# Performance work log

Hardware: AMD Instinct MI355X
Metric: run time of the kernel (lower is better)

Reference implementation:

```python
import jax, jax.numpy as jnp
import numpy as np

N_EMBED = 1024
EMBED_DIM = 64
BETA = 0.25


def setup_inputs() -> dict:
    key = jax.random.key(0)
    k1, k2 = jax.random.split(key)
    x = jax.random.normal(k1, (32, EMBED_DIM, 64, 64), dtype=jnp.float32)  # NCHW, C == embed_dim
    embed = jax.random.uniform(
        k2, (N_EMBED, EMBED_DIM), dtype=jnp.float32,
        minval=-1.0 / N_EMBED, maxval=1.0 / N_EMBED,
    )
    return {"x": x, "embed": embed}


def reference(x, embed):
    # NCHW -> NHWC, flatten spatial+batch to rows of embed_dim
    z = jnp.transpose(x, (0, 2, 3, 1))                      # [B,H,W,D]
    zf = z.reshape(-1, EMBED_DIM)                           # [N,D]
    # squared L2 distance to every codeword: ||z||^2 + ||e||^2 - 2 z.e
    dist = (
        jnp.sum(zf * zf, axis=1, keepdims=True)
        + jnp.sum(embed * embed, axis=1)
        - 2.0 * zf @ embed.T
    )                                                       # [N, n_embed]
    idx = jnp.argmin(dist, axis=1)                          # [N]
    # one-hot @ embed == direct gather (same math, no scatter/matmul)
    z_q = embed[idx].reshape(z.shape)                       # [B,H,W,D]
    sg = jax.lax.stop_gradient
    loss = jnp.mean((sg(z_q) - z) ** 2) + BETA * jnp.mean((z_q - sg(z)) ** 2)
    # straight-through estimator
    z_q = z + sg(z_q - z)
    z_q = jnp.transpose(z_q, (0, 3, 1, 2))                  # back to NCHW
    return (z_q, loss)
```

## Files before the change

### kernel.cpp

```cpp
#include <hip/hip_runtime.h>


#define TOTAL_ELEMS 8388608
#define LOSS_SCALE (1.25f / 8388608.f)

typedef float  f32x4  __attribute__((ext_vector_type(4)));
typedef unsigned int u32x4 __attribute__((ext_vector_type(4)));
typedef long   longx2 __attribute__((ext_vector_type(2)));

static __device__ __forceinline__ void gload_lds16(const void* g, void* l) {
    __builtin_amdgcn_global_load_lds(
        (const __attribute__((address_space(1))) void*)g,
        (__attribute__((address_space(3))) void*)l,
        16, 0, 0);
}

static __device__ __forceinline__ unsigned int umax(unsigned int a, unsigned int b) {
    return a > b ? a : b;
}

__global__ void vq_prep(const float* __restrict__ embed,
                        unsigned char* __restrict__ eb,
                        float* __restrict__ c0,
                        float* __restrict__ loss_slot) {
    int t   = blockIdx.x * 256 + threadIdx.x;
    int row = t >> 2, qd = t & 3;
    const float* s0 = embed + row * 64 + qd * 8;
    const float* s1 = embed + row * 64 + 32 + qd * 8;
    f32x4 v0 = *(const f32x4*)s0, v1 = *(const f32x4*)(s0 + 4);
    f32x4 w0 = *(const f32x4*)s1, w1 = *(const f32x4*)(s1 + 4);
    float s = v0[0]*v0[0] + v0[1]*v0[1] + v0[2]*v0[2] + v0[3]*v0[3]
            + v1[0]*v1[0] + v1[1]*v1[1] + v1[2]*v1[2] + v1[3]*v1[3]
            + w0[0]*w0[0] + w0[1]*w0[1] + w0[2]*w0[2] + w0[3]*w0[3]
            + w1[0]*w1[0] + w1[1]*w1[1] + w1[2]*w1[2] + w1[3]*w1[3];
    unsigned int d0 = 0, d1 = 0, d2 = 0, d3 = 0;
    d0 = __builtin_amdgcn_cvt_pk_fp8_f32(v0[0]*1024.f, v0[1]*1024.f, d0, false);
    d0 = __builtin_amdgcn_cvt_pk_fp8_f32(v0[2]*1024.f, v0[3]*1024.f, d0, true);
    d1 = __builtin_amdgcn_cvt_pk_fp8_f32(v1[0]*1024.f, v1[1]*1024.f, d1, false);
    d1 = __builtin_amdgcn_cvt_pk_fp8_f32(v1[2]*1024.f, v1[3]*1024.f, d1, true);
    d2 = __builtin_amdgcn_cvt_pk_fp8_f32(w0[0]*1024.f, w0[1]*1024.f, d2, false);
    d2 = __builtin_amdgcn_cvt_pk_fp8_f32(w0[2]*1024.f, w0[3]*1024.f, d2, true);
    d3 = __builtin_amdgcn_cvt_pk_fp8_f32(w1[0]*1024.f, w1[1]*1024.f, d3, false);
    d3 = __builtin_amdgcn_cvt_pk_fp8_f32(w1[2]*1024.f, w1[3]*1024.f, d3, true);
    u32x4 o = {d0, d1, d2, d3};
    *(u32x4*)((char*)eb + row * 64 + qd * 16) = o;
    s += __shfl_xor(s, 1);
    s += __shfl_xor(s, 2);
    if (qd == 0) c0[row] = 64.f - 512.f * s;
    if (t == 0) *loss_slot = 0.f;
}

__global__ __launch_bounds__(256, 2) void vq_main(
    const float* __restrict__ x,
    const float* __restrict__ embed,
    const unsigned char* __restrict__ eb,
    const float* __restrict__ c0,
    float* __restrict__ out,
    float* __restrict__ loss) {

    __shared__ __align__(16) unsigned char cb[65536];
    __shared__ __align__(16) float c0l[1024];
    __shared__ float lpart[4];

    const int t    = threadIdx.x;
    const int wv   = t >> 6, lane = t & 63;
    const int l15  = lane & 15, lq = lane >> 4;

    const int blk = blockIdx.x;
    const int b   = blk >> 4;
    const int h0  = (blk & 15) * 4;
    const size_t xbase = (size_t)b * 262144 + (size_t)h0 * 64;

    const char* ebp = (const char*)eb;

#pragma unroll
    for (int s = 0; s < 16; s++)
        gload_lds16(ebp + s * 4096 + t * 16, &cb[s * 4096 + t * 16]);

    *(f32x4*)(c0l + t * 4) = *(const f32x4*)(c0 + t * 4);

    float part = 0.f;
    long bfr[4][2];
#pragma unroll
    for (int nt = 0; nt < 4; nt++) {
#pragma unroll
        for (int kh = 0; kh < 2; kh++) {
            unsigned int dw[2];
#pragma unroll
            for (int p = 0; p < 2; p++) {
                float f[4];
#pragma unroll
                for (int j = 0; j < 4; j++) {
                    f[j] = x[xbase + (size_t)(kh * 32 + lq * 8 + p * 4 + j) * 4096
                             + (size_t)wv * 64 + nt * 16 + l15];
                    part += f[j] * f[j];
                }
                unsigned int r = 0;
                r = __builtin_amdgcn_cvt_pk_fp8_f32(f[0], f[1], r, false);
                r = __builtin_amdgcn_cvt_pk_fp8_f32(f[2], f[3], r, true);
                dw[p] = r;
            }
            bfr[nt][kh] = (long)(((unsigned long long)dw[1] << 32) | dw[0]);
        }
    }
    __syncthreads();

    unsigned int key[4] = {0u, 0u, 0u, 0u};
    const unsigned char* abase = &cb[l15 * 64 + lq * 16];
    const float* cbase = c0l + lq * 4;
#pragma unroll 8
    for (int mt = 0; mt < 64; mt++) {
        longx2 av = *(const longx2*)(abase + mt * 1024);
        f32x4 c0v = *(const f32x4*)(cbase + mt * 16);
        const int invm = 1023 - mt * 16 - lq * 4;
#pragma unroll
        for (int nt = 0; nt < 4; nt++) {
            f32x4 acc = __builtin_amdgcn_mfma_f32_16x16x32_fp8_fp8(
                av[0], bfr[nt][0], c0v, 0, 0, 0);
            acc = __builtin_amdgcn_mfma_f32_16x16x32_fp8_fp8(
                av[1], bfr[nt][1], acc, 0, 0, 0);
            unsigned int k0 = (__float_as_uint(acc[0]) & 0xFFFFFC00u) | (unsigned int)(invm);
            unsigned int k1 = (__float_as_uint(acc[1]) & 0xFFFFFC00u) | (unsigned int)(invm - 1);
            unsigned int k2 = (__float_as_uint(acc[2]) & 0xFFFFFC00u) | (unsigned int)(invm - 2);
            unsigned int k3 = (__float_as_uint(acc[3]) & 0xFFFFFC00u) | (unsigned int)(invm - 3);
            key[nt] = umax(key[nt], umax(umax(k0, k1), umax(k2, k3)));
        }
    }

#pragma unroll
    for (int nt = 0; nt < 4; nt++) {
        unsigned int k = key[nt];
        unsigned int o = (unsigned int)__shfl_xor((int)k, 16); k = umax(k, o);
        o = (unsigned int)__shfl_xor((int)k, 32);              k = umax(k, o);
        key[nt] = k;
        part -= (1.f / 2048.f) * __uint_as_float(k & 0xFFFFFC00u);
    }

    unsigned int klo = (lane & 16) ? key[1] : key[0];
    unsigned int khi = (lane & 16) ? key[3] : key[2];
    unsigned int ks  = (lane & 32) ? khi : klo;
    const int idx = 1023 - (int)(ks & 1023u);

#pragma unroll
    for (int off = 1; off < 64; off <<= 1) part += __shfl_xor(part, off);
    if (lane == 0) lpart[wv] = part;

    const float* erow = embed + idx * 64;
    float* orow = out + xbase + (size_t)wv * 64 + lane;
#pragma unroll
    for (int c4 = 0; c4 < 16; c4++) {
        f32x4 ev = *(const f32x4*)(erow + c4 * 4);
#pragma unroll
        for (int j = 0; j < 4; j++)
            orow[(size_t)(c4 * 4 + j) * 4096] = ev[j];
    }

    __syncthreads();
    if (t == 0) {
        atomicAdd(loss, (lpart[0] + lpart[1] + lpart[2] + lpart[3] + 32.0f) * LOSS_SCALE);
    }
}

extern "C" void kernel_launch(void* const* d_in, const int* in_sizes, int n_in,
                              void* d_out, int out_size, void* d_ws, size_t ws_size,
                              hipStream_t stream) {
    const float* x     = (const float*)d_in[0];
    const float* embed = (const float*)d_in[1];
    unsigned char* eb  = (unsigned char*)d_ws;
    float* c0          = (float*)((char*)d_ws + 65536);
    float* out  = (float*)d_out;
    float* loss = out + TOTAL_ELEMS;

    vq_prep<<<16, 256, 0, stream>>>(embed, eb, c0, loss);
    vq_main<<<512, 256, 0, stream>>>(x, embed, eb, c0, out, loss);
}
```

Before: 37.06 us.

## Use 512-thread blocks and swap MFMA operands so codewords map to columns

Doubles the threads per block to 512, so each wave handles 32 positions instead of 64 while the block still shares one 64KB LDS codebook. The MFMA operand order is swapped so positions become rows and codewords become columns. The argmin then reduces across the 16 lanes with xor shuffles instead of across rows and quads. Indices go through shared memory, and the gather/write is split so each half-wave writes 32 channels. This adds an extra block barrier and more shuffle work, and relies on launch bounds of 4 blocks per CU to hold occupancy.

```diff
diff --git a/kernel.cpp b/kernel.cpp
--- a/kernel.cpp
+++ b/kernel.cpp
@@ -50,7 +50,7 @@
     if (t == 0) *loss_slot = 0.f;
 }
 
-__global__ __launch_bounds__(256, 2) void vq_main(
+__global__ __launch_bounds__(512, 4) void vq_main(
     const float* __restrict__ x,
     const float* __restrict__ embed,
     const unsigned char* __restrict__ eb,
@@ -60,7 +60,8 @@
 
     __shared__ __align__(16) unsigned char cb[65536];
     __shared__ __align__(16) float c0l[1024];
-    __shared__ float lpart[4];
+    __shared__ int   idxf[256];
+    __shared__ float lpart[8];
 
     const int t    = threadIdx.x;
     const int wv   = t >> 6, lane = t & 63;
@@ -70,19 +71,20 @@
     const int b   = blk >> 4;
     const int h0  = (blk & 15) * 4;
     const size_t xbase = (size_t)b * 262144 + (size_t)h0 * 64;
+    const int rowoff = (wv >> 1) * 64 + (wv & 1) * 32;
 
     const char* ebp = (const char*)eb;
 
 #pragma unroll
-    for (int s = 0; s < 16; s++)
-        gload_lds16(ebp + s * 4096 + t * 16, &cb[s * 4096 + t * 16]);
+    for (int s = 0; s < 8; s++)
+        gload_lds16(ebp + s * 8192 + t * 16, &cb[s * 8192 + t * 16]);
 
-    *(f32x4*)(c0l + t * 4) = *(const f32x4*)(c0 + t * 4);
+    if (t < 256) *(f32x4*)(c0l + t * 4) = *(const f32x4*)(c0 + t * 4);
 
     float part = 0.f;
-    long bfr[4][2];
+    long bfr[2][2];
 #pragma unroll
-    for (int nt = 0; nt < 4; nt++) {
+    for (int nt = 0; nt < 2; nt++) {
 #pragma unroll
         for (int kh = 0; kh < 2; kh++) {
             unsigned int dw[2];
@@ -92,7 +94,7 @@
 #pragma unroll
                 for (int j = 0; j < 4; j++) {
                     f[j] = x[xbase + (size_t)(kh * 32 + lq * 8 + p * 4 + j) * 4096
-                             + (size_t)wv * 64 + nt * 16 + l15];
+                             + (size_t)rowoff + nt * 16 + l15];
                     part += f[j] * f[j];
                 }
                 unsigned int r = 0;
@@ -105,59 +107,75 @@
     }
     __syncthreads();
 
-    unsigned int key[4] = {0u, 0u, 0u, 0u};
-    const unsigned char* abase = &cb[l15 * 64 + lq * 16];
-    const float* cbase = c0l + lq * 4;
+    unsigned int key[8];
+#pragma unroll
+    for (int s = 0; s < 8; s++) key[s] = 0u;
+    const unsigned char* bbase = &cb[l15 * 64 + lq * 16];
+    const float* cbase = c0l + l15;
+    const unsigned int invb = (unsigned int)(1023 - l15);
 #pragma unroll 8
     for (int mt = 0; mt < 64; mt++) {
-        longx2 av = *(const longx2*)(abase + mt * 1024);
-        f32x4 c0v = *(const f32x4*)(cbase + mt * 16);
-        const int invm = 1023 - mt * 16 - lq * 4;
+        longx2 bv = *(const longx2*)(bbase + mt * 1024);
+        float c0s = cbase[mt * 16];
+        f32x4 c0v = {c0s, c0s, c0s, c0s};
+        const unsigned int inv = invb - mt * 16;
 #pragma unroll
-        for (int nt = 0; nt < 4; nt++) {
+        for (int nt = 0; nt < 2; nt++) {
             f32x4 acc = __builtin_amdgcn_mfma_f32_16x16x32_fp8_fp8(
-                av[0], bfr[nt][0], c0v, 0, 0, 0);
+                bfr[nt][0], bv[0], c0v, 0, 0, 0);
             acc = __builtin_amdgcn_mfma_f32_16x16x32_fp8_fp8(
-                av[1], bfr[nt][1], acc, 0, 0, 0);
-            unsigned int k0 = (__float_as_uint(acc[0]) & 0xFFFFFC00u) | (unsigned int)(invm);
-            unsigned int k1 = (__float_as_uint(acc[1]) & 0xFFFFFC00u) | (unsigned int)(invm - 1);
-            unsigned int k2 = (__float_as_uint(acc[2]) & 0xFFFFFC00u) | (unsigned int)(invm - 2);
-            unsigned int k3 = (__float_as_uint(acc[3]) & 0xFFFFFC00u) | (unsigned int)(invm - 3);
-            key[nt] = umax(key[nt], umax(umax(k0, k1), umax(k2, k3)));
+                bfr[nt][1], bv[1], acc, 0, 0, 0);
+#pragma unroll
+            for (int r = 0; r < 4; r++) {
+                unsigned int k2 = (__float_as_uint(acc[r]) & 0xFFFFFC00u) | inv;
+                key[nt * 4 + r] = umax(key[nt * 4 + r], k2);
+            }
         }
     }
 
 #pragma unroll
-    for (int nt = 0; nt < 4; nt++) {
-        unsigned int k = key[nt];
-        unsigned int o = (unsigned int)__shfl_xor((int)k, 16); k = umax(k, o);
-        o = (unsigned int)__shfl_xor((int)k, 32);              k = umax(k, o);
-        key[nt] = k;
-        part -= (1.f / 2048.f) * __uint_as_float(k & 0xFFFFFC00u);
+    for (int s = 0; s < 8; s++) {
+        unsigned int k = key[s];
+        k = umax(k, (unsigned int)__shfl_xor((int)k, 1));
+        k = umax(k, (unsigned int)__shfl_xor((int)k, 2));
+        k = umax(k, (unsigned int)__shfl_xor((int)k, 4));
+        k = umax(k, (unsigned int)__shfl_xor((int)k, 8));
+        key[s] = k;
     }
-
-    unsigned int klo = (lane & 16) ? key[1] : key[0];
-    unsigned int khi = (lane & 16) ? key[3] : key[2];
-    unsigned int ks  = (lane & 32) ? khi : klo;
-    const int idx = 1023 - (int)(ks & 1023u);
+    if (l15 == 0) {
+#pragma unroll
+        for (int nt = 0; nt < 2; nt++) {
+#pragma unroll
+            for (int r = 0; r < 4; r++) {
+                unsigned int k = key[nt * 4 + r];
+                idxf[rowoff + nt * 16 + lq * 4 + r] = 1023 - (int)(k & 1023u);
+                part -= (1.f / 512.f) * __uint_as_float(k & 0xFFFFFC00u);
+            }
+        }
+    }
 
 #pragma unroll
     for (int off = 1; off < 64; off <<= 1) part += __shfl_xor(part, off);
     if (lane == 0) lpart[wv] = part;
+    __syncthreads();
 
-    const float* erow = embed + idx * 64;
-    float* orow = out + xbase + (size_t)wv * 64 + lane;
+    const int ch0 = (lane >> 5) * 32;
+    const int pos = lane & 31;
+    const int idx = idxf[rowoff + pos];
+    const float* erow = embed + idx * 64 + ch0;
+    float* orow = out + xbase + (size_t)rowoff + pos + (size_t)ch0 * 4096;
 #pragma unroll
-    for (int c4 = 0; c4 < 16; c4++) {
+    for (int c4 = 0; c4 < 8; c4++) {
         f32x4 ev = *(const f32x4*)(erow + c4 * 4);
 #pragma unroll
         for (int j = 0; j < 4; j++)
             orow[(size_t)(c4 * 4 + j) * 4096] = ev[j];
     }
 
-    __syncthreads();
     if (t == 0) {
-        atomicAdd(loss, (lpart[0] + lpart[1] + lpart[2] + lpart[3] + 32.0f) * LOSS_SCALE);
+        float s = lpart[0] + lpart[1] + lpart[2] + lpart[3]
+                + lpart[4] + lpart[5] + lpart[6] + lpart[7];
+        atomicAdd(loss, (s + 32.0f) * LOSS_SCALE);
     }
 }
 
@@ -172,5 +190,5 @@
     float* loss = out + TOTAL_ELEMS;
 
     vq_prep<<<16, 256, 0, stream>>>(embed, eb, c0, loss);
-    vq_main<<<512, 256, 0, stream>>>(x, embed, eb, c0, out, loss);
+    vq_main<<<512, 512, 0, stream>>>(x, embed, eb, c0, out, loss);
 }
```

Result: no change. 37.53 us (+1.3%).

## Split codebook across waves per block, read fragments from global instead of LDS

Applied to the files above, without the earlier changes.

Each block now handles one 64-pixel row instead of four. The four waves split the 1024 codewords four ways and combine their argmin keys through shared memory, in place of each wave scanning the full codebook held in LDS. The prep kernel writes the fp8 codebook directly in MFMA fragment order, so the main kernel loads A operands straight from global/L2 without the 64KB LDS staging. The grid grows to 2048 blocks and launch bounds are removed. This drops LDS occupancy limits and per-block codebook staging, but every wave redundantly loads the same x tile and adds two block barriers plus a cross-wave reduction.

```diff
diff --git a/kernel.cpp b/kernel.cpp
--- a/kernel.cpp
+++ b/kernel.cpp
@@ -4,16 +4,7 @@
 #define TOTAL_ELEMS 8388608
 #define LOSS_SCALE (1.25f / 8388608.f)
 
-typedef float  f32x4  __attribute__((ext_vector_type(4)));
-typedef unsigned int u32x4 __attribute__((ext_vector_type(4)));
-typedef long   longx2 __attribute__((ext_vector_type(2)));
-
-static __device__ __forceinline__ void gload_lds16(const void* g, void* l) {
-    __builtin_amdgcn_global_load_lds(
-        (const __attribute__((address_space(1))) void*)g,
-        (__attribute__((address_space(3))) void*)l,
-        16, 0, 0);
-}
+typedef float f32x4 __attribute__((ext_vector_type(4)));
 
 static __device__ __forceinline__ unsigned int umax(unsigned int a, unsigned int b) {
     return a > b ? a : b;
@@ -25,6 +16,7 @@
                         float* __restrict__ loss_slot) {
     int t   = blockIdx.x * 256 + threadIdx.x;
     int row = t >> 2, qd = t & 3;
+    int mt  = row >> 4, rl = row & 15;
     const float* s0 = embed + row * 64 + qd * 8;
     const float* s1 = embed + row * 64 + 32 + qd * 8;
     f32x4 v0 = *(const f32x4*)s0, v1 = *(const f32x4*)(s0 + 4);
@@ -42,15 +34,18 @@
     d2 = __builtin_amdgcn_cvt_pk_fp8_f32(w0[2]*1024.f, w0[3]*1024.f, d2, true);
     d3 = __builtin_amdgcn_cvt_pk_fp8_f32(w1[0]*1024.f, w1[1]*1024.f, d3, false);
     d3 = __builtin_amdgcn_cvt_pk_fp8_f32(w1[2]*1024.f, w1[3]*1024.f, d3, true);
-    u32x4 o = {d0, d1, d2, d3};
-    *(u32x4*)((char*)eb + row * 64 + qd * 16) = o;
+    unsigned long long g0 = (unsigned long long)d0 | ((unsigned long long)d1 << 32);
+    unsigned long long g1 = (unsigned long long)d2 | ((unsigned long long)d3 << 32);
+    char* tb = (char*)eb + mt * 1024 + (qd * 16 + rl) * 8;
+    *(unsigned long long*)(tb)       = g0;
+    *(unsigned long long*)(tb + 512) = g1;
     s += __shfl_xor(s, 1);
     s += __shfl_xor(s, 2);
     if (qd == 0) c0[row] = 64.f - 512.f * s;
     if (t == 0) *loss_slot = 0.f;
 }
 
-__global__ __launch_bounds__(256, 2) void vq_main(
+__global__ void vq_main(
     const float* __restrict__ x,
     const float* __restrict__ embed,
     const unsigned char* __restrict__ eb,
@@ -58,26 +53,16 @@
     float* __restrict__ out,
     float* __restrict__ loss) {
 
-    __shared__ __align__(16) unsigned char cb[65536];
-    __shared__ __align__(16) float c0l[1024];
-    __shared__ float lpart[4];
+    __shared__ unsigned int wkey[4][64];
+    __shared__ int idxf[64];
 
     const int t    = threadIdx.x;
     const int wv   = t >> 6, lane = t & 63;
     const int l15  = lane & 15, lq = lane >> 4;
 
     const int blk = blockIdx.x;
-    const int b   = blk >> 4;
-    const int h0  = (blk & 15) * 4;
-    const size_t xbase = (size_t)b * 262144 + (size_t)h0 * 64;
-
-    const char* ebp = (const char*)eb;
-
-#pragma unroll
-    for (int s = 0; s < 16; s++)
-        gload_lds16(ebp + s * 4096 + t * 16, &cb[s * 4096 + t * 16]);
-
-    *(f32x4*)(c0l + t * 4) = *(const f32x4*)(c0 + t * 4);
+    const int b   = blk >> 6, h = blk & 63;
+    const size_t xbase = (size_t)b * 262144 + (size_t)h * 64;
 
     float part = 0.f;
     long bfr[4][2];
@@ -92,7 +77,7 @@
 #pragma unroll
                 for (int j = 0; j < 4; j++) {
                     f[j] = x[xbase + (size_t)(kh * 32 + lq * 8 + p * 4 + j) * 4096
-                             + (size_t)wv * 64 + nt * 16 + l15];
+                             + nt * 16 + l15];
                     part += f[j] * f[j];
                 }
                 unsigned int r = 0;
@@ -103,22 +88,29 @@
             bfr[nt][kh] = (long)(((unsigned long long)dw[1] << 32) | dw[0]);
         }
     }
-    __syncthreads();
+    float zsq = 0.f;
+    if (wv == 0) {
+#pragma unroll
+        for (int off = 1; off < 64; off <<= 1) part += __shfl_xor(part, off);
+        zsq = part;
+    }
 
     unsigned int key[4] = {0u, 0u, 0u, 0u};
-    const unsigned char* abase = &cb[l15 * 64 + lq * 16];
-    const float* cbase = c0l + lq * 4;
-#pragma unroll 8
-    for (int mt = 0; mt < 64; mt++) {
-        longx2 av = *(const longx2*)(abase + mt * 1024);
-        f32x4 c0v = *(const f32x4*)(cbase + mt * 16);
-        const int invm = 1023 - mt * 16 - lq * 4;
+    const char* ebq = (const char*)eb + wv * 16384 + lane * 8;
+    const float* c0q = c0 + wv * 256 + lq * 4;
+    const int invq = 1023 - wv * 256 - lq * 4;
+#pragma unroll 4
+    for (int m = 0; m < 16; m++) {
+        long a0 = *(const long*)(ebq + m * 1024);
+        long a1 = *(const long*)(ebq + m * 1024 + 512);
+        f32x4 c0v = *(const f32x4*)(c0q + m * 16);
+        const int invm = invq - m * 16;
 #pragma unroll
         for (int nt = 0; nt < 4; nt++) {
             f32x4 acc = __builtin_amdgcn_mfma_f32_16x16x32_fp8_fp8(
-                av[0], bfr[nt][0], c0v, 0, 0, 0);
+                a0, bfr[nt][0], c0v, 0, 0, 0);
             acc = __builtin_amdgcn_mfma_f32_16x16x32_fp8_fp8(
-                av[1], bfr[nt][1], acc, 0, 0, 0);
+                a1, bfr[nt][1], acc, 0, 0, 0);
             unsigned int k0 = (__float_as_uint(acc[0]) & 0xFFFFFC00u) | (unsigned int)(invm);
             unsigned int k1 = (__float_as_uint(acc[1]) & 0xFFFFFC00u) | (unsigned int)(invm - 1);
             unsigned int k2 = (__float_as_uint(acc[2]) & 0xFFFFFC00u) | (unsigned int)(invm - 2);
@@ -130,35 +122,36 @@
 #pragma unroll
     for (int nt = 0; nt < 4; nt++) {
         unsigned int k = key[nt];
-        unsigned int o = (unsigned int)__shfl_xor((int)k, 16); k = umax(k, o);
-        o = (unsigned int)__shfl_xor((int)k, 32);              k = umax(k, o);
-        key[nt] = k;
-        part -= (1.f / 2048.f) * __uint_as_float(k & 0xFFFFFC00u);
+        k = umax(k, (unsigned int)__shfl_xor((int)k, 16));
+        k = umax(k, (unsigned int)__shfl_xor((int)k, 32));
+        if (lane < 16) wkey[wv][nt * 16 + lane] = k;
     }
+    __syncthreads();
 
-    unsigned int klo = (lane & 16) ? key[1] : key[0];
-    unsigned int khi = (lane & 16) ? key[3] : key[2];
-    unsigned int ks  = (lane & 32) ? khi : klo;
-    const int idx = 1023 - (int)(ks & 1023u);
+    float la = 0.f;
+    if (t < 64) {
+        unsigned int k = umax(umax(wkey[0][t], wkey[1][t]),
+                              umax(wkey[2][t], wkey[3][t]));
+        idxf[t] = 1023 - (int)(k & 1023u);
+        la = -(1.f / 512.f) * __uint_as_float(k & 0xFFFFFC00u);
+#pragma unroll
+        for (int off = 1; off < 64; off <<= 1) la += __shfl_xor(la, off);
+    }
+    __syncthreads();
 
+    const int idx = idxf[lane];
+    const float* erow = embed + idx * 64 + wv * 16;
+    float* obase = out + xbase + (size_t)(wv * 16) * 4096 + lane;
 #pragma unroll
-    for (int off = 1; off < 64; off <<= 1) part += __shfl_xor(part, off);
-    if (lane == 0) lpart[wv] = part;
-
-    const float* erow = embed + idx * 64;
-    float* orow = out + xbase + (size_t)wv * 64 + lane;
-#pragma unroll
-    for (int c4 = 0; c4 < 16; c4++) {
+    for (int c4 = 0; c4 < 4; c4++) {
         f32x4 ev = *(const f32x4*)(erow + c4 * 4);
 #pragma unroll
         for (int j = 0; j < 4; j++)
-            orow[(size_t)(c4 * 4 + j) * 4096] = ev[j];
+            obase[(size_t)(c4 * 4 + j) * 4096] = ev[j];
     }
 
-    __syncthreads();
-    if (t == 0) {
-        atomicAdd(loss, (lpart[0] + lpart[1] + lpart[2] + lpart[3] + 32.0f) * LOSS_SCALE);
-    }
+    if (t == 0)
+        atomicAdd(loss, (zsq + la + 8.0f) * LOSS_SCALE);
 }
 
 extern "C" void kernel_launch(void* const* d_in, const int* in_sizes, int n_in,
@@ -172,5 +165,5 @@
     float* loss = out + TOTAL_ELEMS;
 
     vq_prep<<<16, 256, 0, stream>>>(embed, eb, c0, loss);
-    vq_main<<<512, 256, 0, stream>>>(x, embed, eb, c0, out, loss);
+    vq_main<<<2048, 256, 0, stream>>>(x, embed, eb, c0, out, loss);
 }
```

Result: slower. 45.95 us (+24.0%).

## Fuse codebook prep into main kernel with padded LDS rows and 512-thread blocks

Applied to the files above, without the earlier changes.

Removes the separate prep kernel: each block now reads the fp32 codebook, computes the norms and fp8-quantizes it straight into LDS, using 72-byte padded rows to avoid bank conflicts. Blocks grow to 512 threads (8 waves), each wave handling 32 positions instead of 64, which halves the per-wave MFMA work and the register footprint. The loss slot is zeroed with a memset instead. In exchange, all 512 blocks redo the codebook conversion, which adds redundant global reads and ALU work per block.

```diff
diff --git a/kernel.cpp b/kernel.cpp
--- a/kernel.cpp
+++ b/kernel.cpp
@@ -3,64 +3,27 @@
 
 #define TOTAL_ELEMS 8388608
 #define LOSS_SCALE (1.25f / 8388608.f)
+#define ROWB 72
 
-typedef float  f32x4  __attribute__((ext_vector_type(4)));
+typedef float  f32x4 __attribute__((ext_vector_type(4)));
 typedef unsigned int u32x4 __attribute__((ext_vector_type(4)));
-typedef long   longx2 __attribute__((ext_vector_type(2)));
-
-static __device__ __forceinline__ void gload_lds16(const void* g, void* l) {
-    __builtin_amdgcn_global_load_lds(
-        (const __attribute__((address_space(1))) void*)g,
-        (__attribute__((address_space(3))) void*)l,
-        16, 0, 0);
-}
 
 static __device__ __forceinline__ unsigned int umax(unsigned int a, unsigned int b) {
     return a > b ? a : b;
 }
-
-__global__ void vq_prep(const float* __restrict__ embed,
-                        unsigned char* __restrict__ eb,
-                        float* __restrict__ c0,
-                        float* __restrict__ loss_slot) {
-    int t   = blockIdx.x * 256 + threadIdx.x;
-    int row = t >> 2, qd = t & 3;
-    const float* s0 = embed + row * 64 + qd * 8;
-    const float* s1 = embed + row * 64 + 32 + qd * 8;
-    f32x4 v0 = *(const f32x4*)s0, v1 = *(const f32x4*)(s0 + 4);
-    f32x4 w0 = *(const f32x4*)s1, w1 = *(const f32x4*)(s1 + 4);
-    float s = v0[0]*v0[0] + v0[1]*v0[1] + v0[2]*v0[2] + v0[3]*v0[3]
-            + v1[0]*v1[0] + v1[1]*v1[1] + v1[2]*v1[2] + v1[3]*v1[3]
-            + w0[0]*w0[0] + w0[1]*w0[1] + w0[2]*w0[2] + w0[3]*w0[3]
-            + w1[0]*w1[0] + w1[1]*w1[1] + w1[2]*w1[2] + w1[3]*w1[3];
-    unsigned int d0 = 0, d1 = 0, d2 = 0, d3 = 0;
-    d0 = __builtin_amdgcn_cvt_pk_fp8_f32(v0[0]*1024.f, v0[1]*1024.f, d0, false);
-    d0 = __builtin_amdgcn_cvt_pk_fp8_f32(v0[2]*1024.f, v0[3]*1024.f, d0, true);
-    d1 = __builtin_amdgcn_cvt_pk_fp8_f32(v1[0]*1024.f, v1[1]*1024.f, d1, false);
-    d1 = __builtin_amdgcn_cvt_pk_fp8_f32(v1[2]*1024.f, v1[3]*1024.f, d1, true);
-    d2 = __builtin_amdgcn_cvt_pk_fp8_f32(w0[0]*1024.f, w0[1]*1024.f, d2, false);
-    d2 = __builtin_amdgcn_cvt_pk_fp8_f32(w0[2]*1024.f, w0[3]*1024.f, d2, true);
-    d3 = __builtin_amdgcn_cvt_pk_fp8_f32(w1[0]*1024.f, w1[1]*1024.f, d3, false);
-    d3 = __builtin_amdgcn_cvt_pk_fp8_f32(w1[2]*1024.f, w1[3]*1024.f, d3, true);
-    u32x4 o = {d0, d1, d2, d3};
-    *(u32x4*)((char*)eb + row * 64 + qd * 16) = o;
-    s += __shfl_xor(s, 1);
-    s += __shfl_xor(s, 2);
-    if (qd == 0) c0[row] = 64.f - 512.f * s;
-    if (t == 0) *loss_slot = 0.f;
+static __device__ __forceinline__ float dot4(f32x4 v) {
+    return v[0]*v[0] + v[1]*v[1] + v[2]*v[2] + v[3]*v[3];
 }
 
-__global__ __launch_bounds__(256, 2) void vq_main(
+__global__ void vq_main(
     const float* __restrict__ x,
     const float* __restrict__ embed,
-    const unsigned char* __restrict__ eb,
-    const float* __restrict__ c0,
     float* __restrict__ out,
     float* __restrict__ loss) {
 
-    __shared__ __align__(16) unsigned char cb[65536];
+    __shared__ __align__(16) unsigned char cb[1024 * ROWB];
     __shared__ __align__(16) float c0l[1024];
-    __shared__ float lpart[4];
+    __shared__ float lpart[8];
 
     const int t    = threadIdx.x;
     const int wv   = t >> 6, lane = t & 63;
@@ -70,19 +33,39 @@
     const int b   = blk >> 4;
     const int h0  = (blk & 15) * 4;
     const size_t xbase = (size_t)b * 262144 + (size_t)h0 * 64;
-
-    const char* ebp = (const char*)eb;
+    const int rowoff = (wv >> 1) * 64 + (wv & 1) * 32;
 
 #pragma unroll
-    for (int s = 0; s < 16; s++)
-        gload_lds16(ebp + s * 4096 + t * 16, &cb[s * 4096 + t * 16]);
-
-    *(f32x4*)(c0l + t * 4) = *(const f32x4*)(c0 + t * 4);
+    for (int rr = 0; rr < 2; rr++) {
+        const int r = t + rr * 512;
+        const float* er = embed + r * 64;
+        float s = 0.f;
+#pragma unroll
+        for (int p = 0; p < 4; p++) {
+            f32x4 v0 = *(const f32x4*)(er + p * 16);
+            f32x4 v1 = *(const f32x4*)(er + p * 16 + 4);
+            f32x4 v2 = *(const f32x4*)(er + p * 16 + 8);
+            f32x4 v3 = *(const f32x4*)(er + p * 16 + 12);
+            s += dot4(v0) + dot4(v1) + dot4(v2) + dot4(v3);
+            unsigned int d0 = 0, d1 = 0, d2 = 0, d3 = 0;
+            d0 = __builtin_amdgcn_cvt_pk_fp8_f32(v0[0]*1024.f, v0[1]*1024.f, d0, false);
+            d0 = __builtin_amdgcn_cvt_pk_fp8_f32(v0[2]*1024.f, v0[3]*1024.f, d0, true);
+            d1 = __builtin_amdgcn_cvt_pk_fp8_f32(v1[0]*1024.f, v1[1]*1024.f, d1, false);
+            d1 = __builtin_amdgcn_cvt_pk_fp8_f32(v1[2]*1024.f, v1[3]*1024.f, d1, true);
+            d2 = __builtin_amdgcn_cvt_pk_fp8_f32(v2[0]*1024.f, v2[1]*1024.f, d2, false);
+            d2 = __builtin_amdgcn_cvt_pk_fp8_f32(v2[2]*1024.f, v2[3]*1024.f, d2, true);
+            d3 = __builtin_amdgcn_cvt_pk_fp8_f32(v3[0]*1024.f, v3[1]*1024.f, d3, false);
+            d3 = __builtin_amdgcn_cvt_pk_fp8_f32(v3[2]*1024.f, v3[3]*1024.f, d3, true);
+            u32x4 q = {d0, d1, d2, d3};
+            *(u32x4*)(&cb[r * ROWB + p * 16]) = q;
+        }
+        c0l[r] = 64.f - 512.f * s;
+    }
 
     float part = 0.f;
-    long bfr[4][2];
+    long bfr[2][2];
 #pragma unroll
-    for (int nt = 0; nt < 4; nt++) {
+    for (int nt = 0; nt < 2; nt++) {
 #pragma unroll
         for (int kh = 0; kh < 2; kh++) {
             unsigned int dw[2];
@@ -92,7 +75,7 @@
 #pragma unroll
                 for (int j = 0; j < 4; j++) {
                     f[j] = x[xbase + (size_t)(kh * 32 + lq * 8 + p * 4 + j) * 4096
-                             + (size_t)wv * 64 + nt * 16 + l15];
+                             + (size_t)rowoff + nt * 16 + l15];
                     part += f[j] * f[j];
                 }
                 unsigned int r = 0;
@@ -105,20 +88,21 @@
     }
     __syncthreads();
 
-    unsigned int key[4] = {0u, 0u, 0u, 0u};
-    const unsigned char* abase = &cb[l15 * 64 + lq * 16];
+    unsigned int key[2] = {0u, 0u};
+    const unsigned char* bbase = &cb[l15 * ROWB + lq * 8];
     const float* cbase = c0l + lq * 4;
 #pragma unroll 8
     for (int mt = 0; mt < 64; mt++) {
-        longx2 av = *(const longx2*)(abase + mt * 1024);
+        long a0 = *(const long*)(bbase + mt * 16 * ROWB);
+        long a1 = *(const long*)(bbase + mt * 16 * ROWB + 32);
         f32x4 c0v = *(const f32x4*)(cbase + mt * 16);
         const int invm = 1023 - mt * 16 - lq * 4;
 #pragma unroll
-        for (int nt = 0; nt < 4; nt++) {
+        for (int nt = 0; nt < 2; nt++) {
             f32x4 acc = __builtin_amdgcn_mfma_f32_16x16x32_fp8_fp8(
-                av[0], bfr[nt][0], c0v, 0, 0, 0);
+                a0, bfr[nt][0], c0v, 0, 0, 0);
             acc = __builtin_amdgcn_mfma_f32_16x16x32_fp8_fp8(
-                av[1], bfr[nt][1], acc, 0, 0, 0);
+                a1, bfr[nt][1], acc, 0, 0, 0);
             unsigned int k0 = (__float_as_uint(acc[0]) & 0xFFFFFC00u) | (unsigned int)(invm);
             unsigned int k1 = (__float_as_uint(acc[1]) & 0xFFFFFC00u) | (unsigned int)(invm - 1);
             unsigned int k2 = (__float_as_uint(acc[2]) & 0xFFFFFC00u) | (unsigned int)(invm - 2);
@@ -128,7 +112,7 @@
     }
 
 #pragma unroll
-    for (int nt = 0; nt < 4; nt++) {
+    for (int nt = 0; nt < 2; nt++) {
         unsigned int k = key[nt];
         unsigned int o = (unsigned int)__shfl_xor((int)k, 16); k = umax(k, o);
         o = (unsigned int)__shfl_xor((int)k, 32);              k = umax(k, o);
@@ -136,19 +120,19 @@
         part -= (1.f / 2048.f) * __uint_as_float(k & 0xFFFFFC00u);
     }
 
-    unsigned int klo = (lane & 16) ? key[1] : key[0];
-    unsigned int khi = (lane & 16) ? key[3] : key[2];
-    unsigned int ks  = (lane & 32) ? khi : klo;
+    unsigned int ks = ((lane >> 4) & 1) ? key[1] : key[0];
     const int idx = 1023 - (int)(ks & 1023u);
 
 #pragma unroll
     for (int off = 1; off < 64; off <<= 1) part += __shfl_xor(part, off);
     if (lane == 0) lpart[wv] = part;
 
-    const float* erow = embed + idx * 64;
-    float* orow = out + xbase + (size_t)wv * 64 + lane;
+    const int ch0 = (lane >> 5) * 32;
+    const int pos = lane & 31;
+    const float* erow = embed + idx * 64 + ch0;
+    float* orow = out + xbase + (size_t)rowoff + pos + (size_t)ch0 * 4096;
 #pragma unroll
-    for (int c4 = 0; c4 < 16; c4++) {
+    for (int c4 = 0; c4 < 8; c4++) {
         f32x4 ev = *(const f32x4*)(erow + c4 * 4);
 #pragma unroll
         for (int j = 0; j < 4; j++)
@@ -157,7 +141,9 @@
 
     __syncthreads();
     if (t == 0) {
-        atomicAdd(loss, (lpart[0] + lpart[1] + lpart[2] + lpart[3] + 32.0f) * LOSS_SCALE);
+        float s = lpart[0] + lpart[1] + lpart[2] + lpart[3]
+                + lpart[4] + lpart[5] + lpart[6] + lpart[7];
+        atomicAdd(loss, (s + 32.0f) * LOSS_SCALE);
     }
 }
 
@@ -166,11 +152,9 @@
                               hipStream_t stream) {
     const float* x     = (const float*)d_in[0];
     const float* embed = (const float*)d_in[1];
-    unsigned char* eb  = (unsigned char*)d_ws;
-    float* c0          = (float*)((char*)d_ws + 65536);
     float* out  = (float*)d_out;
     float* loss = out + TOTAL_ELEMS;
 
-    vq_prep<<<16, 256, 0, stream>>>(embed, eb, c0, loss);
-    vq_main<<<512, 256, 0, stream>>>(x, embed, eb, c0, out, loss);
+    hipMemsetAsync(loss, 0, sizeof(float), stream);
+    vq_main<<<512, 512, 0, stream>>>(x, embed, out, loss);
 }
```

New measurement: 47.22 us. +27.4%, slower.
